# Optimization experiments

Measured on AMD Instinct MI355X. Metric: run time of the kernel, lower is better.

## Reference

```python
import jax, jax.numpy as jnp
import numpy as np


def setup_inputs() -> dict:
    key = jax.random.key(0)
    ks = jax.random.split(key, 4)
    B, T, D, U = 32, 1024, 1024, 1024
    x = jax.random.normal(ks[0], (B, T, D), dtype=jnp.float32)
    W = jax.random.normal(ks[1], (D, 4 * U), dtype=jnp.float32) * (1.0 / np.sqrt(D))
    b = jnp.zeros((4 * U,), dtype=jnp.float32)
    Vr = jax.random.normal(ks[2], (U,), dtype=jnp.float32) * 0.1
    Vf = jax.random.normal(ks[3], (U,), dtype=jnp.float32) * 0.1
    h0 = jnp.zeros((B, U), dtype=jnp.float32)
    c0 = jnp.zeros((B, U), dtype=jnp.float32)
    return {"x": x, "h0": h0, "c0": c0, "W": W, "b": b, "Vr": Vr, "Vf": Vf}


def _sru(x, h0, c0, W, b, Vr, Vf):
    B, T, D = x.shape
    U = Vr.shape[0]
    # Batched matmul across all timesteps, then sequential elementwise scan.
    g = jnp.einsum('btd,dk->btk', x, W) + b            # [B, T, 4U]
    g = jnp.moveaxis(g, 1, 0)                          # [T, B, 4U]
    g1, g2, g3, g4 = jnp.split(g, 4, axis=-1)          # each [T, B, U]

    def step(c_, gs):
        a1, a2, a3, a4 = gs
        f = jax.nn.sigmoid(a1 + Vf * c_)
        c = f * c_ + (1.0 - f) * a2
        r = jax.nn.sigmoid(a3 + Vr * c_)
        h = r * c + (1.0 - r) * a4
        return c, h

    c_last, hs = jax.lax.scan(step, c0, (g1, g2, g3, g4))
    return jnp.moveaxis(hs, 0, 1)                      # [B, T, U]


def reference(x, h0, c0, W, b, Vr, Vf):
    return _sru(x, h0, c0, W, b, Vr, Vf)
```

## Files before the change

### kernel.cpp

```cpp
#include <hip/hip_runtime.h>
#include <cstdint>
#include <cstddef>

typedef short short8 __attribute__((ext_vector_type(8)));
typedef short s16x4 __attribute__((ext_vector_type(4)));
typedef float f32x4 __attribute__((ext_vector_type(4)));

typedef const __attribute__((address_space(1))) void* gas_ptr;
typedef __attribute__((address_space(3))) void* las_ptr;

__device__ __forceinline__ unsigned short f2bf(float f) {
    unsigned int u = __float_as_uint(f);
    u += 0x7fffu + ((u >> 16) & 1u);
    return (unsigned short)(u >> 16);
}
__device__ __forceinline__ float bf2f(unsigned short s) {
    return __uint_as_float(((unsigned int)s) << 16);
}
__device__ __forceinline__ float sigmoid_f(float z) {
    return __builtin_amdgcn_rcpf(1.0f + __expf(-z));
}
__device__ __forceinline__ void async_copy16(const void* gp, void* lp) {
    __builtin_amdgcn_global_load_lds((gas_ptr)gp, (las_ptr)lp, 16, 0, 0);
}

__global__ __launch_bounds__(256) void cvt_x_kernel(const float* __restrict__ in,
                                                    unsigned short* __restrict__ out) {
    size_t i = ((size_t)blockIdx.x * 256 + threadIdx.x) * 8;
    float4 v0 = *(const float4*)(in + i);
    float4 v1 = *(const float4*)(in + i + 4);
    short8 o;
    o[0]=(short)f2bf(v0.x); o[1]=(short)f2bf(v0.y); o[2]=(short)f2bf(v0.z); o[3]=(short)f2bf(v0.w);
    o[4]=(short)f2bf(v1.x); o[5]=(short)f2bf(v1.y); o[6]=(short)f2bf(v1.z); o[7]=(short)f2bf(v1.w);
    *(short8*)(out + i) = o;
}

__global__ __launch_bounds__(256) void cvt_w_kernel(const float* __restrict__ W,
                                                    unsigned short* __restrict__ Wt) {
    __shared__ unsigned short tile[64][65];
    int bk = blockIdx.x >> 6, bn = blockIdx.x & 63;
    int k0 = bk * 64, n0 = bn * 64;
    int t = threadIdx.x;
    int cr = t >> 6;
    int cc = t & 63;
#pragma unroll
    for (int i = 0; i < 16; ++i) {
        int row = i * 4 + cr;
        tile[row][cc] = f2bf(W[(size_t)(k0 + row) * 4096 + n0 + cc]);
    }
    __syncthreads();
#pragma unroll
    for (int i = 0; i < 16; ++i) {
        int nrow = i * 4 + cr;
        Wt[(size_t)(n0 + nrow) * 1024 + k0 + cc] = tile[cc][nrow];
    }
}

__global__ __launch_bounds__(256, 2) void gemm_kernel(const unsigned short* __restrict__ A,
                                                      const unsigned short* __restrict__ Bt,
                                                      const float* __restrict__ bias,
                                                      unsigned short* __restrict__ gT) {
    __shared__ __align__(16) unsigned short As[128 * 64];
    __shared__ __align__(16) unsigned short Bs[128 * 64];

    int bid = blockIdx.x;
    int band = bid >> 8;
    int r = bid & 255;
    int mt = band * 8 + (r >> 5);
    int nt = r & 31;
    int m0 = mt * 128, n0 = nt * 128;

    int tidx = threadIdx.x;
    int lane = tidx & 63, wv = tidx >> 6;
    int wm = wv >> 1, wn = wv & 1;
    int l15 = lane & 15, quad = lane >> 4;

    f32x4 acc[4][4] = {};

    for (int k0 = 0; k0 < 1024; k0 += 64) {
        __syncthreads();
#pragma unroll
        for (int i = 0; i < 4; ++i) {
            int ci = (wv * 4 + i) * 64 + lane;
            int row = ci >> 3, cc = ci & 7;
            int sc = (cc ^ (row & 7)) << 3;
            const unsigned short* ga = A + (size_t)(m0 + row) * 1024 + k0 + sc;
            async_copy16(ga, (char*)As + (wv * 4 + i) * 1024);
            const unsigned short* gb = Bt + (size_t)(n0 + row) * 1024 + k0 + sc;
            async_copy16(gb, (char*)Bs + (wv * 4 + i) * 1024);
        }
        __syncthreads();
#pragma unroll
        for (int kt = 0; kt < 2; ++kt) {
            short8 af[4], bf[4];
#pragma unroll
            for (int mt2 = 0; mt2 < 4; ++mt2) {
                int row = wm * 64 + mt2 * 16 + l15;
                int kc = kt * 4 + quad;
                af[mt2] = *(const short8*)((const char*)As + row * 128 + ((kc ^ (row & 7)) << 4));
            }
#pragma unroll
            for (int nt2 = 0; nt2 < 4; ++nt2) {
                int rown = wn * 64 + nt2 * 16 + l15;
                int kc = kt * 4 + quad;
                bf[nt2] = *(const short8*)((const char*)Bs + rown * 128 + ((kc ^ (rown & 7)) << 4));
            }
#pragma unroll
            for (int mt2 = 0; mt2 < 4; ++mt2)
#pragma unroll
                for (int nt2 = 0; nt2 < 4; ++nt2)
                    acc[mt2][nt2] = __builtin_amdgcn_mfma_f32_16x16x32_bf16(
                        af[mt2], bf[nt2], acc[mt2][nt2], 0, 0, 0);
        }
    }

#pragma unroll
    for (int mt2 = 0; mt2 < 4; ++mt2) {
        int mbase = m0 + wm * 64 + mt2 * 16 + quad * 4;
        int b_ = mbase >> 10, t_ = mbase & 1023;
#pragma unroll
        for (int nt2 = 0; nt2 < 4; ++nt2) {
            int n = n0 + wn * 64 + nt2 * 16 + l15;
            int gate = n >> 10, u = n & 1023;
            float bv = bias[n];
            s16x4 pk;
            pk[0] = (short)f2bf(acc[mt2][nt2][0] + bv);
            pk[1] = (short)f2bf(acc[mt2][nt2][1] + bv);
            pk[2] = (short)f2bf(acc[mt2][nt2][2] + bv);
            pk[3] = (short)f2bf(acc[mt2][nt2][3] + bv);
            size_t off = ((((size_t)(t_ >> 3) * 32 + (size_t)b_) * 4 + (size_t)gate) << 13)
                         + ((size_t)u << 3) + (size_t)(t_ & 7);
            *(s16x4*)(gT + off) = pk;
        }
    }
}

__global__ __launch_bounds__(64) void scan_kernel(const unsigned short* __restrict__ gT,
                                                  const float* __restrict__ c0,
                                                  const float* __restrict__ Vr,
                                                  const float* __restrict__ Vf,
                                                  float* __restrict__ h) {
    int tid = blockIdx.x * 64 + threadIdx.x;
    int b = tid >> 10, u = tid & 1023;
    const size_t TBS = (size_t)32 * 4 * 8192;
    const unsigned short* p1 = gT + ((size_t)b * 4) * 8192 + ((size_t)u << 3);
    const unsigned short* p2 = p1 + 8192;
    const unsigned short* p3 = p2 + 8192;
    const unsigned short* p4 = p3 + 8192;
    float* hb = h + ((size_t)b << 20) + u;
    float c = c0[(b << 10) + u];
    float vf = Vf[u], vr = Vr[u];

    short8 r1[4], r2[4], r3[4], r4[4];
#pragma unroll
    for (int i = 0; i < 4; ++i) {
        r1[i] = *(const short8*)(p1 + (size_t)i * TBS);
        r2[i] = *(const short8*)(p2 + (size_t)i * TBS);
        r3[i] = *(const short8*)(p3 + (size_t)i * TBS);
        r4[i] = *(const short8*)(p4 + (size_t)i * TBS);
    }
    for (int tb = 0; tb < 128; tb += 4) {
#pragma unroll
        for (int s = 0; s < 4; ++s) {
            short8 a1 = r1[s], a2 = r2[s], a3 = r3[s], a4 = r4[s];
            int tpn = tb + 4 + s;
            if (tpn < 128) {
                size_t o = (size_t)tpn * TBS;
                r1[s] = *(const short8*)(p1 + o);
                r2[s] = *(const short8*)(p2 + o);
                r3[s] = *(const short8*)(p3 + o);
                r4[s] = *(const short8*)(p4 + o);
            }
            int t0 = (tb + s) * 8;
#pragma unroll
            for (int i = 0; i < 8; ++i) {
                float x1 = bf2f((unsigned short)a1[i]);
                float x2 = bf2f((unsigned short)a2[i]);
                float x3 = bf2f((unsigned short)a3[i]);
                float x4 = bf2f((unsigned short)a4[i]);
                float f  = sigmoid_f(x1 + vf * c);
                float cn = fmaf(f, c - x2, x2);
                float rr = sigmoid_f(x3 + vr * c);
                float hv = fmaf(rr, cn - x4, x4);
                c = cn;
                hb[(size_t)(t0 + i) << 10] = hv;
            }
        }
    }
}

extern "C" void kernel_launch(void* const* d_in, const int* in_sizes, int n_in,
                              void* d_out, int out_size, void* d_ws, size_t ws_size,
                              hipStream_t stream) {
    const float* x  = (const float*)d_in[0];
    const float* c0 = (const float*)d_in[2];
    const float* W  = (const float*)d_in[3];
    const float* b  = (const float*)d_in[4];
    const float* Vr = (const float*)d_in[5];
    const float* Vf = (const float*)d_in[6];
    float* h = (float*)d_out;

    char* ws = (char*)d_ws;
    unsigned short* xb = (unsigned short*)ws;
    unsigned short* wt = (unsigned short*)(ws + (size_t)67108864);
    unsigned short* gT = (unsigned short*)(ws + (size_t)75497472);

    cvt_x_kernel<<<16384, 256, 0, stream>>>(x, xb);
    cvt_w_kernel<<<1024, 256, 0, stream>>>(W, wt);
    gemm_kernel<<<8192, 256, 0, stream>>>(xb, wt, b, gT);
    scan_kernel<<<512, 64, 0, stream>>>(gT, c0, Vr, Vf, h);
}
```

Before: 559.1 us.

## Warp-specialize scan: producer wave streams gates into LDS ring buffer

The scan kernel now runs two waves per block. One producer wave issues async global-to-LDS copies of the gate slices into an 8-deep ring buffer, and one consumer wave runs the sequential recurrence, with the two synchronised by s_barrier and vmcnt waits. The aim is to hide gate-load latency behind the scan by prefetching deeper than the old register prefetch allowed. In exchange it adds one barrier per timestep block and relies on hand-set vmcnt counts being correct.

```diff
diff --git a/kernel.cpp b/kernel.cpp
--- a/kernel.cpp
+++ b/kernel.cpp
@@ -135,43 +135,69 @@
     }
 }
 
-__global__ __launch_bounds__(64) void scan_kernel(const unsigned short* __restrict__ gT,
-                                                  const float* __restrict__ c0,
-                                                  const float* __restrict__ Vr,
-                                                  const float* __restrict__ Vf,
-                                                  float* __restrict__ h) {
-    int tid = blockIdx.x * 64 + threadIdx.x;
-    int b = tid >> 10, u = tid & 1023;
-    const size_t TBS = (size_t)32 * 4 * 8192;
-    const unsigned short* p1 = gT + ((size_t)b * 4) * 8192 + ((size_t)u << 3);
-    const unsigned short* p2 = p1 + 8192;
-    const unsigned short* p3 = p2 + 8192;
-    const unsigned short* p4 = p3 + 8192;
-    float* hb = h + ((size_t)b << 20) + u;
-    float c = c0[(b << 10) + u];
-    float vf = Vf[u], vr = Vr[u];
-
-    short8 r1[4], r2[4], r3[4], r4[4];
-#pragma unroll
-    for (int i = 0; i < 4; ++i) {
-        r1[i] = *(const short8*)(p1 + (size_t)i * TBS);
-        r2[i] = *(const short8*)(p2 + (size_t)i * TBS);
-        r3[i] = *(const short8*)(p3 + (size_t)i * TBS);
-        r4[i] = *(const short8*)(p4 + (size_t)i * TBS);
-    }
-    for (int tb = 0; tb < 128; tb += 4) {
-#pragma unroll
-        for (int s = 0; s < 4; ++s) {
-            short8 a1 = r1[s], a2 = r2[s], a3 = r3[s], a4 = r4[s];
-            int tpn = tb + 4 + s;
-            if (tpn < 128) {
-                size_t o = (size_t)tpn * TBS;
-                r1[s] = *(const short8*)(p1 + o);
-                r2[s] = *(const short8*)(p2 + o);
-                r3[s] = *(const short8*)(p3 + o);
-                r4[s] = *(const short8*)(p4 + o);
-            }
-            int t0 = (tb + s) * 8;
+__global__ __launch_bounds__(128) void scan_kernel(const unsigned short* __restrict__ gT,
+                                                   const float* __restrict__ c0,
+                                                   const float* __restrict__ Vr,
+                                                   const float* __restrict__ Vf,
+                                                   float* __restrict__ h) {
+    __shared__ __align__(16) unsigned short sbuf[8 * 2048];
+
+    const int NT = 128;
+    const int D = 8;
+    int blk = blockIdx.x;
+    int b = blk >> 4;
+    int u0 = (blk & 15) << 6;
+    int tid = threadIdx.x;
+    int wv = tid >> 6;
+    int lane = tid & 63;
+
+    if (wv == 0) {
+        size_t base = ((size_t)b * 4) * 8192 + ((size_t)(u0 + lane) << 3);
+        const unsigned short* pg0 = gT + base;
+        const unsigned short* pg1 = pg0 + 8192;
+        const unsigned short* pg2 = pg1 + 8192;
+        const unsigned short* pg3 = pg2 + 8192;
+#pragma unroll
+        for (int g = 0; g < D - 1; ++g) {
+            char* ld = (char*)sbuf + (g & 7) * 4096;
+            size_t o = (size_t)g << 20;
+            async_copy16(pg0 + o, ld);
+            async_copy16(pg1 + o, ld + 1024);
+            async_copy16(pg2 + o, ld + 2048);
+            async_copy16(pg3 + o, ld + 3072);
+        }
+        for (int j = 0; j < NT; ++j) {
+            if (j < NT - (D - 2)) {
+                asm volatile("s_waitcnt vmcnt(24)" ::: "memory");
+            } else {
+                asm volatile("s_waitcnt vmcnt(0)" ::: "memory");
+            }
+            __builtin_amdgcn_s_barrier();
+            int g = j + D - 1;
+            if (g < NT) {
+                char* ld = (char*)sbuf + (g & 7) * 4096;
+                size_t o = (size_t)g << 20;
+                async_copy16(pg0 + o, ld);
+                async_copy16(pg1 + o, ld + 1024);
+                async_copy16(pg2 + o, ld + 2048);
+                async_copy16(pg3 + o, ld + 3072);
+            }
+        }
+    } else {
+        int u = u0 + lane;
+        float c = c0[(b << 10) + u];
+        float vf = Vf[u], vr = Vr[u];
+        float* hb = h + ((size_t)b << 20) + u;
+        const unsigned short* ls = sbuf + (size_t)lane * 8;
+        for (int j = 0; j < NT; ++j) {
+            __builtin_amdgcn_s_barrier();
+            asm volatile("" ::: "memory");
+            int so = (j & 7) * 2048;
+            short8 a1 = *(const short8*)(ls + so);
+            short8 a2 = *(const short8*)(ls + so + 512);
+            short8 a3 = *(const short8*)(ls + so + 1024);
+            short8 a4 = *(const short8*)(ls + so + 1536);
+            int t0 = j * 8;
 #pragma unroll
             for (int i = 0; i < 8; ++i) {
                 float x1 = bf2f((unsigned short)a1[i]);
@@ -208,5 +234,5 @@
     cvt_x_kernel<<<16384, 256, 0, stream>>>(x, xb);
     cvt_w_kernel<<<1024, 256, 0, stream>>>(W, wt);
     gemm_kernel<<<8192, 256, 0, stream>>>(xb, wt, b, gT);
-    scan_kernel<<<512, 64, 0, stream>>>(gT, c0, Vr, Vf, h);
-}
+    scan_kernel<<<512, 128, 0, stream>>>(gT, c0, Vr, Vf, h);
+}
```

Measured after the change: 550.3 us. Within noise of the previous version (-1.6%).
